# Kernel tuning notes

Measured on AMD Instinct MI355X. Metric: run time of the kernel, lower is better.

## Reference

```python
import jax, jax.numpy as jnp
import numpy as np

SCALE = 1.0 / 16.0      # spatial scale: image coords -> feature-map coords (stride-16 backbone)
OUT = 7                 # roi_pool_outsize
RATIO = 2               # sampling_ratio
NUM_CLASSES = 21
HID = 1024
SCORE_THRESH = 0.05
NMS_THRESH = 0.5
DET = 100               # detections_per_img
MIN_SIZE = 0.01
LOG_MAX = float(np.log(1000.0 / 16.0))  # standard bbox decode dw/dh clamp


def _bilinear(feat, ys, xs):
    # feat [C,H,W]; ys [Py], xs [Px] -> [C,Py,Px] (torchvision roi_align interpolation, aligned=False)
    C, H, W = feat.shape
    vy = (ys > -1.0) & (ys < H)
    vx = (xs > -1.0) & (xs < W)
    y = jnp.clip(ys, 0.0, H - 1.0)
    x = jnp.clip(xs, 0.0, W - 1.0)
    y0 = jnp.floor(y).astype(jnp.int32)
    x0 = jnp.floor(x).astype(jnp.int32)
    y1 = jnp.minimum(y0 + 1, H - 1)
    x1 = jnp.minimum(x0 + 1, W - 1)
    ly = (y - y0)[:, None]
    lx = (x - x0)[None, :]
    f00 = feat[:, y0[:, None], x0[None, :]]
    f01 = feat[:, y0[:, None], x1[None, :]]
    f10 = feat[:, y1[:, None], x0[None, :]]
    f11 = feat[:, y1[:, None], x1[None, :]]
    val = (f00 * (1.0 - ly) * (1.0 - lx) + f01 * (1.0 - ly) * lx
           + f10 * ly * (1.0 - lx) + f11 * ly * lx)
    return val * (vy[:, None] & vx[None, :])


def _roi_align(features, boxes, bidx):
    # features [N,C,H,W], boxes [R,4] (image coords), bidx [R] -> [R,C,OUT,OUT]
    N, C, H, W = features.shape
    b = boxes * SCALE
    rw = jnp.maximum(b[:, 2] - b[:, 0], 1.0)
    rh = jnp.maximum(b[:, 3] - b[:, 1], 1.0)
    bw = rw / OUT
    bh = rh / OUT
    # per-bin sample offsets: (ph + (i+0.5)/ratio) for ph in [0,OUT), i in [0,RATIO)
    g = (jnp.arange(OUT, dtype=jnp.float32)[:, None]
         + (jnp.arange(RATIO, dtype=jnp.float32)[None, :] + 0.5) / RATIO).reshape(-1)  # [OUT*RATIO]
    ys = b[:, 1][:, None] + g[None, :] * bh[:, None]  # [R, OUT*RATIO]
    xs = b[:, 0][:, None] + g[None, :] * bw[:, None]
    vals = jax.vmap(lambda i, yr, xr: _bilinear(features[i], yr, xr))(bidx, ys, xs)  # [R,C,P,P]
    R = boxes.shape[0]
    return vals.reshape(R, C, OUT, RATIO, OUT, RATIO).mean(axis=(3, 5))


def _decode(deltas, props):
    # deltas [R,K,4], props [R,4]; weights (10,10,5,5) as in the module
    pw = props[:, 2] - props[:, 0]
    ph = props[:, 3] - props[:, 1]
    pcx = props[:, 0] + 0.5 * pw
    pcy = props[:, 1] + 0.5 * ph
    dx = deltas[..., 0] / 10.0
    dy = deltas[..., 1] / 10.0
    dw = jnp.minimum(deltas[..., 2] / 5.0, LOG_MAX)
    dh = jnp.minimum(deltas[..., 3] / 5.0, LOG_MAX)
    cx = dx * pw[:, None] + pcx[:, None]
    cy = dy * ph[:, None] + pcy[:, None]
    w = jnp.exp(dw) * pw[:, None]
    h = jnp.exp(dh) * ph[:, None]
    return jnp.stack([cx - 0.5 * w, cy - 0.5 * h, cx + 0.5 * w, cy + 0.5 * h], axis=-1)


def _per_image(scores, boxes, img):
    # scores [S,K], boxes [S,K,4]. Drop background class, flatten, filter, class-aware NMS, top-DET.
    S, K = scores.shape
    sc = scores[:, 1:].reshape(-1)                 # [M]
    bx = boxes[:, 1:, :].reshape(-1, 4)            # [M,4]
    lb = jnp.broadcast_to(jnp.arange(1, K, dtype=jnp.int32)[None, :], (S, K - 1)).reshape(-1)
    wv = bx[:, 2] - bx[:, 0]
    hv = bx[:, 3] - bx[:, 1]
    valid = (sc > SCORE_THRESH) & (wv >= MIN_SIZE) & (hv >= MIN_SIZE)
    live0 = jnp.where(valid, sc, -1.0)
    # batched_nms via per-class coordinate offsets
    nb = bx + (lb.astype(bx.dtype) * (img + 1.0))[:, None]
    areas = (nb[:, 2] - nb[:, 0]) * (nb[:, 3] - nb[:, 1])

    def step(live, _):
        i = jnp.argmax(live)
        s = live[i]
        b = nb[i]
        xx1 = jnp.maximum(b[0], nb[:, 0])
        yy1 = jnp.maximum(b[1], nb[:, 1])
        xx2 = jnp.minimum(b[2], nb[:, 2])
        yy2 = jnp.minimum(b[3], nb[:, 3])
        inter = jnp.maximum(xx2 - xx1, 0.0) * jnp.maximum(yy2 - yy1, 0.0)
        area_i = (b[2] - b[0]) * (b[3] - b[1])
        iou = inter / (area_i + areas - inter + 1e-9)
        live = jnp.where(iou > NMS_THRESH, -1.0, live)  # also suppresses i itself (iou=1)
        return live, (i, s)

    _, (idxs, svals) = jax.lax.scan(step, live0, None, length=DET)
    keep = svals > SCORE_THRESH
    out_boxes = jnp.where(keep[:, None], bx[idxs], 0.0)
    out_scores = jnp.where(keep, svals, 0.0)
    out_labels = jnp.where(keep, lb[idxs], 0)
    return out_boxes, out_scores, out_labels


def _forward(features, proposals, w1, b1, w2, b2, wc, bc, wb, bb, image_size):
    N, C, H, W = features.shape
    S = proposals.shape[1]
    props = proposals.reshape(-1, 4)
    bidx = jnp.repeat(jnp.arange(N), S)
    feats = _roi_align(features, props, bidx)          # [R,C,7,7]
    x = feats.reshape(N * S, -1)                       # [R, C*49]
    h = jax.nn.relu(x @ w1 + b1)
    h = jax.nn.relu(h @ w2 + b2)
    cls = h @ wc + bc                                  # [R,K]
    deltas = (h @ wb + bb).reshape(N * S, NUM_CLASSES, 4)
    scores = jax.nn.softmax(cls, axis=-1)
    boxes = _decode(deltas, props)                     # [R,K,4]
    img = float(image_size)
    boxes = jnp.clip(boxes, 0.0, img)                  # square image -> clip both coords to [0,img]
    scores = scores.reshape(N, S, NUM_CLASSES)
    boxes = boxes.reshape(N, S, NUM_CLASSES, 4)
    return jax.vmap(lambda s, bx: _per_image(s, bx, img))(scores, boxes)


def setup_inputs() -> dict:
    key = jax.random.key(0)
    ks = jax.random.split(key, 12)
    N, S, C, H, W = 2, 512, 512, 50, 50
    IMG = 800
    features = jax.random.normal(ks[0], (N, C, H, W), jnp.float32)
    x1 = jax.random.uniform(ks[1], (N, S)) * (IMG - 80.0)
    y1 = jax.random.uniform(ks[2], (N, S)) * (IMG - 80.0)
    x2 = jnp.minimum(x1 + 16.0 + jax.random.uniform(ks[3], (N, S)) * 180.0, float(IMG))
    y2 = jnp.minimum(y1 + 16.0 + jax.random.uniform(ks[4], (N, S)) * 180.0, float(IMG))
    proposals = jnp.stack([x1, y1, x2, y2], axis=-1)
    D = C * OUT * OUT  # 25088
    w1 = jax.random.normal(ks[5], (D, HID), jnp.float32) * 0.01
    b1 = jnp.zeros((HID,), jnp.float32)
    w2 = jax.random.normal(ks[6], (HID, HID), jnp.float32) * 0.02
    b2 = jnp.zeros((HID,), jnp.float32)
    wc = jax.random.normal(ks[7], (HID, NUM_CLASSES), jnp.float32) * 0.05
    bc = jnp.zeros((NUM_CLASSES,), jnp.float32)
    wb = jax.random.normal(ks[8], (HID, NUM_CLASSES * 4), jnp.float32) * 0.02
    bb = jnp.zeros((NUM_CLASSES * 4,), jnp.float32)
    return {"features": features, "proposals": proposals, "w1": w1, "b1": b1,
            "w2": w2, "b2": b2, "wc": wc, "bc": bc, "wb": wb, "bb": bb,
            "image_size": IMG}


def reference(features, proposals, w1, b1, w2, b2, wc, bc, wb, bb, image_size):
    boxes, scores, labels = _forward(features, proposals, w1, b1, w2, b2, wc, bc, wb, bb, image_size)
    return boxes, scores, labels
```

## Files before the change

kernel.cpp:

```cpp
#include <hip/hip_runtime.h>
#include <cmath>

#define NIMG 2
#define SPROP 512
#define NROI 1024
#define CCH 512
#define FH 50
#define FW 50
#define K1 25088
#define HID 1024
#define NCLS 21
#define NDET 100
#define IMGSZ 800.0f
#define LOGMAX 4.135166556742356f
#define MCAND 10240
#define ZSPLIT 8
#define KCHUNK 3136
#define ZSPLIT2 8
#define KCHUNK2 128

typedef unsigned short u16;
typedef __attribute__((ext_vector_type(8))) short short8;
typedef __attribute__((ext_vector_type(4))) float f32x4;
typedef __attribute__((ext_vector_type(16))) float f32x16;

__device__ __forceinline__ u16 f2bf(float x) {
  unsigned int u = __float_as_uint(x);
  u += 0x7fffu + ((u >> 16) & 1u);
  return (u16)(u >> 16);
}
__device__ __forceinline__ float bf2f(u16 h) {
  return __uint_as_float(((unsigned int)h) << 16);
}

template <bool BF16OUT>
__global__ __launch_bounds__(256) void roi_kernel(
    const float* __restrict__ feat, const float* __restrict__ props,
    float* __restrict__ X, u16* __restrict__ Xhi, u16* __restrict__ Xlo) {
  const int r = blockIdx.x;
  const int n = r >> 9;
  const int tid = threadIdx.x;
  __shared__ float tile[32 * 273 + 16];
  __shared__ float4 ymeta[14];
  __shared__ float4 xmeta[14];
  __shared__ int smin[2];

  const float p0 = props[r * 4 + 0] * 0.0625f;
  const float p1 = props[r * 4 + 1] * 0.0625f;
  const float p2 = props[r * 4 + 2] * 0.0625f;
  const float p3 = props[r * 4 + 3] * 0.0625f;
  const float bw = fmaxf(p2 - p0, 1.0f) / 7.0f;
  const float bh = fmaxf(p3 - p1, 1.0f) / 7.0f;

  if (tid < 14) {
    const int j = tid;
    const float g = (float)(j >> 1) + ((float)(j & 1) + 0.5f) * 0.5f;
    const float y = p1 + g * bh;
    const float vy = (y > -1.0f && y < (float)FH) ? 0.5f : 0.0f;
    const float yc = fminf(fmaxf(y, 0.0f), (float)(FH - 1));
    const int y0 = (int)floorf(yc);
    const int y1 = min(y0 + 1, FH - 1);
    const float ly = yc - (float)y0;
    const float yc0 = fminf(fmaxf(p1 + 0.25f * bh, 0.0f), (float)(FH - 1));
    const int ymin = (int)floorf(yc0);
    float4 m;
    m.x = __int_as_float((y0 - ymin) * 17);
    m.y = __int_as_float((y1 - ymin) * 17);
    m.z = (1.0f - ly) * vy;
    m.w = ly * vy;
    ymeta[j] = m;
    if (j == 0) smin[0] = ymin;
  } else if (tid >= 16 && tid < 30) {
    const int j = tid - 16;
    const float g = (float)(j >> 1) + ((float)(j & 1) + 0.5f) * 0.5f;
    const float x = p0 + g * bw;
    const float vx = (x > -1.0f && x < (float)FW) ? 0.5f : 0.0f;
    const float xc = fminf(fmaxf(x, 0.0f), (float)(FW - 1));
    const int x0 = (int)floorf(xc);
    const int x1 = min(x0 + 1, FW - 1);
    const float lx = xc - (float)x0;
    const float xc0 = fminf(fmaxf(p0 + 0.25f * bw, 0.0f), (float)(FW - 1));
    const int xmin = (int)floorf(xc0);
    const float wx0 = (1.0f - lx) * vx;
    const float wx1 = lx * vx;
    const int d = x1 - x0;
    float4 m;
    m.x = __int_as_float(x0 - xmin);
    m.y = wx0 + (d ? 0.0f : wx1);
    m.z = d ? wx1 : 0.0f;
    m.w = 0.0f;
    xmeta[j] = m;
    if (j == 0) smin[1] = xmin;
  }
  __syncthreads();

  const int ymin = smin[0], xmin = smin[1];
  const float* fb = feat + (size_t)n * CCH * (FH * FW);
  const int gy = min(ymin + (tid >> 4), FH - 1);
  const int gx = min(xmin + (tid & 15), FW - 1);
  const int offp = gy * FW + gx;
  const int wslot = (tid >> 4) * 17 + (tid & 15);
  const int q = tid & 7;
  const int c = tid >> 3;
  const int cb = c * 273;

  float pf[32];
#pragma unroll
  for (int e = 0; e < 32; ++e) pf[e] = fb[(size_t)e * (FH * FW) + offp];

  for (int cc = 0; cc < 16; ++cc) {
#pragma unroll
    for (int e = 0; e < 32; ++e) tile[e * 273 + wslot] = pf[e];
    __syncthreads();
    if (cc < 15) {
      const float* fb2 = fb + (size_t)(cc + 1) * 32 * (FH * FW);
#pragma unroll
      for (int e = 0; e < 32; ++e) pf[e] = fb2[(size_t)e * (FH * FW) + offp];
    }
#pragma unroll
    for (int jj = 0; jj < 7; ++jj) {
      const int s = q + (jj << 3);
      if (s < 49) {
        const int oy = s / 7;
        const int ox = s - oy * 7;
        const float4 ym0 = ymeta[2 * oy];
        const float4 ym1 = ymeta[2 * oy + 1];
        const float4 xm0 = xmeta[2 * ox];
        const float4 xm1 = xmeta[2 * ox + 1];
        float acc = 0.0f;
#pragma unroll
        for (int sy = 0; sy < 2; ++sy) {
          const float4 ym = sy ? ym1 : ym0;
          const int ro0 = cb + __float_as_int(ym.x);
          const int ro1 = cb + __float_as_int(ym.y);
#pragma unroll
          for (int sx = 0; sx < 2; ++sx) {
            const float4 xm = sx ? xm1 : xm0;
            const int px = __float_as_int(xm.x);
            const float a0 = tile[ro0 + px];
            const float a1 = tile[ro0 + px + 1];
            const float b0 = tile[ro1 + px];
            const float b1 = tile[ro1 + px + 1];
            acc += ym.z * (xm.y * a0 + xm.z * a1) +
                   ym.w * (xm.y * b0 + xm.z * b1);
          }
        }
        const size_t k = (size_t)r * K1 + (size_t)(cc * 32 + c) * 49 + s;
        if (BF16OUT) {
          const u16 h = f2bf(acc);
          Xhi[k] = h;
          Xlo[k] = f2bf(acc - bf2f(h));
        } else {
          X[k] = acc;
        }
      }
    }
    __syncthreads();
  }
}

template <int KDIM>
__global__ __launch_bounds__(256) void convw_kernel(
    const float* __restrict__ w, u16* __restrict__ Wh, u16* __restrict__ Wl) {
  __shared__ u16 sh[64][65], sl[64][65];
  const int k0 = blockIdx.x * 64;
  const int n0 = blockIdx.y * 64;
  const int t = threadIdx.x;
#pragma unroll
  for (int e = 0; e < 16; ++e) {
    const int idx = t + e * 256;
    const int kl = idx >> 6, nl = idx & 63;
    const float v = w[(size_t)(k0 + kl) * HID + n0 + nl];
    const u16 h = f2bf(v);
    sh[kl][nl] = h;
    sl[kl][nl] = f2bf(v - bf2f(h));
  }
  __syncthreads();
#pragma unroll
  for (int e = 0; e < 16; ++e) {
    const int idx = t + e * 256;
    const int nl = idx >> 6, kl = idx & 63;
    Wh[(size_t)(n0 + nl) * KDIM + k0 + kl] = sh[kl][nl];
    Wl[(size_t)(n0 + nl) * KDIM + k0 + kl] = sl[kl][nl];
  }
}

template <int KS, int KCH, bool SWZ>
__global__ __launch_bounds__(512, 2) void gemm_mfma_split(
    const u16* __restrict__ Ahg, const u16* __restrict__ Alg,
    const u16* __restrict__ Bhg, const u16* __restrict__ Blg,
    float* __restrict__ CP) {
  __shared__ u16 Ah[128][32], Al[128][32], Bh[256][32], Bl[256][32];
  const int tid = threadIdx.x;
  const int lane = tid & 63;
  const int wv = tid >> 6;
  const int wm = (wv >> 2) << 6;
  const int wn = (wv & 3) << 6;

  int bx = blockIdx.x, by = blockIdx.y, bz = blockIdx.z;
  if (SWZ) {
    const int f = blockIdx.x + ((blockIdx.y + (blockIdx.z << 3)) << 2);
    bz = f & 7;
    const int u = f >> 3;
    bx = u & 3;
    by = u >> 2;
  }
  const int mT = by << 7;
  const int nT = bx << 8;
  const int kz = bz * KCH;
  const int kend = kz + KCH;

  const int sr = tid >> 2;
  const int sq = (tid & 3) << 3;
  const int scw = (((tid & 3) ^ ((sr >> 1) & 3)) << 3);
  const size_t aoff  = (size_t)(mT + sr) * KS + sq;
  const size_t b0off = (size_t)(nT + sr) * KS + sq;
  const size_t b1off = (size_t)(nT + sr + 128) * KS + sq;

  f32x16 acc[2][2];
#pragma unroll
  for (int i = 0; i < 2; ++i)
#pragma unroll
    for (int j = 0; j < 2; ++j)
#pragma unroll
      for (int e = 0; e < 16; ++e) acc[i][j][e] = 0.0f;

  const int fm = lane & 31;
  const int fh = lane >> 5;
  const int vswz = (fm >> 1) & 3;

  uint4 rA  = *(const uint4*)(Ahg + aoff + kz);
  uint4 rL  = *(const uint4*)(Alg + aoff + kz);
  uint4 rB0 = *(const uint4*)(Bhg + b0off + kz);
  uint4 rB1 = *(const uint4*)(Bhg + b1off + kz);
  uint4 rM0 = *(const uint4*)(Blg + b0off + kz);
  uint4 rM1 = *(const uint4*)(Blg + b1off + kz);
  uint4 sA  = *(const uint4*)(Ahg + aoff + kz + 32);
  uint4 sL  = *(const uint4*)(Alg + aoff + kz + 32);
  uint4 sB0 = *(const uint4*)(Bhg + b0off + kz + 32);
  uint4 sB1 = *(const uint4*)(Bhg + b1off + kz + 32);
  uint4 sM0 = *(const uint4*)(Blg + b0off + kz + 32);
  uint4 sM1 = *(const uint4*)(Blg + b1off + kz + 32);

  auto compute = [&]() {
#pragma unroll
    for (int kh = 0; kh < 2; ++kh) {
      const int cA = ((((kh << 1) | fh) ^ vswz) << 3);
      short8 fa_h[2], fa_l[2], fb_h[2], fb_l[2];
#pragma unroll
      for (int t = 0; t < 2; ++t) {
        fa_h[t] = *(const short8*)(&Ah[wm + t * 32 + fm][cA]);
        fa_l[t] = *(const short8*)(&Al[wm + t * 32 + fm][cA]);
        fb_h[t] = *(const short8*)(&Bh[wn + t * 32 + fm][cA]);
        fb_l[t] = *(const short8*)(&Bl[wn + t * 32 + fm][cA]);
      }
#pragma unroll
      for (int ti = 0; ti < 2; ++ti)
#pragma unroll
        for (int tj = 0; tj < 2; ++tj) {
          acc[ti][tj] = __builtin_amdgcn_mfma_f32_32x32x16_bf16(
              fa_h[ti], fb_h[tj], acc[ti][tj], 0, 0, 0);
          acc[ti][tj] = __builtin_amdgcn_mfma_f32_32x32x16_bf16(
              fa_h[ti], fb_l[tj], acc[ti][tj], 0, 0, 0);
          acc[ti][tj] = __builtin_amdgcn_mfma_f32_32x32x16_bf16(
              fa_l[ti], fb_h[tj], acc[ti][tj], 0, 0, 0);
        }
    }
  };

  for (int kb = kz; kb < kend; kb += 64) {
    *(uint4*)(&Ah[sr][scw]) = rA;
    *(uint4*)(&Al[sr][scw]) = rL;
    *(uint4*)(&Bh[sr][scw]) = rB0;
    *(uint4*)(&Bh[sr + 128][scw]) = rB1;
    *(uint4*)(&Bl[sr][scw]) = rM0;
    *(uint4*)(&Bl[sr + 128][scw]) = rM1;
    __syncthreads();
    const int kn1 = (kb + 64 < kend) ? kb + 64 : kz;
    rA  = *(const uint4*)(Ahg + aoff + kn1);
    rL  = *(const uint4*)(Alg + aoff + kn1);
    rB0 = *(const uint4*)(Bhg + b0off + kn1);
    rB1 = *(const uint4*)(Bhg + b1off + kn1);
    rM0 = *(const uint4*)(Blg + b0off + kn1);
    rM1 = *(const uint4*)(Blg + b1off + kn1);
    compute();
    __syncthreads();
    *(uint4*)(&Ah[sr][scw]) = sA;
    *(uint4*)(&Al[sr][scw]) = sL;
    *(uint4*)(&Bh[sr][scw]) = sB0;
    *(uint4*)(&Bh[sr + 128][scw]) = sB1;
    *(uint4*)(&Bl[sr][scw]) = sM0;
    *(uint4*)(&Bl[sr + 128][scw]) = sM1;
    __syncthreads();
    const int kn2 = (kb + 96 < kend) ? kb + 96 : kz;
    sA  = *(const uint4*)(Ahg + aoff + kn2);
    sL  = *(const uint4*)(Alg + aoff + kn2);
    sB0 = *(const uint4*)(Bhg + b0off + kn2);
    sB1 = *(const uint4*)(Bhg + b1off + kn2);
    sM0 = *(const uint4*)(Blg + b0off + kn2);
    sM1 = *(const uint4*)(Blg + b1off + kn2);
    compute();
    __syncthreads();
  }

  float* Cp = CP + (size_t)bz * ((size_t)NROI * HID);
  const int ccol = nT + wn + fm;
  const int rbase = mT + wm + (fh << 2);
#pragma unroll
  for (int ti = 0; ti < 2; ++ti)
#pragma unroll
    for (int tj = 0; tj < 2; ++tj)
#pragma unroll
      for (int rg = 0; rg < 16; ++rg) {
        const int row = rbase + ti * 32 + (rg & 3) + 8 * (rg >> 2);
        Cp[(size_t)row * HID + ccol + tj * 32] = acc[ti][tj][rg];
      }
}

__global__ __launch_bounds__(256) void gemm1_kernel(
    const float* __restrict__ A, const float* __restrict__ B,
    float* __restrict__ CP) {
  __shared__ float As[16][68];
  __shared__ float Bs[16][68];
  const int tid = threadIdx.x;
  const int mTile = blockIdx.y << 6;
  const int nTile = blockIdx.x << 6;
  const int k0 = blockIdx.z * KCHUNK;
  const int ty = tid >> 4, tx = tid & 15;
  const int ar = tid >> 2, ac = (tid & 3) << 2;
  const int br = tid >> 4, bcl = (tid & 15) << 2;
  float acc[4][4] = {};

  for (int kb = k0; kb < k0 + KCHUNK; kb += 16) {
    const float4 av = *(const float4*)(A + (size_t)(mTile + ar) * K1 + kb + ac);
    const float4 bv = *(const float4*)(B + (size_t)(kb + br) * HID + nTile + bcl);
    As[ac + 0][ar] = av.x; As[ac + 1][ar] = av.y;
    As[ac + 2][ar] = av.z; As[ac + 3][ar] = av.w;
    *(float4*)(&Bs[br][bcl]) = bv;
    __syncthreads();
#pragma unroll
    for (int kk = 0; kk < 16; ++kk) {
      const float4 a4 = *(const float4*)(&As[kk][ty << 2]);
      const float4 b4 = *(const float4*)(&Bs[kk][tx << 2]);
      const float aa[4] = {a4.x, a4.y, a4.z, a4.w};
      const float bb4[4] = {b4.x, b4.y, b4.z, b4.w};
#pragma unroll
      for (int i = 0; i < 4; ++i)
#pragma unroll
        for (int j = 0; j < 4; ++j)
          acc[i][j] = fmaf(aa[i], bb4[j], acc[i][j]);
    }
    __syncthreads();
  }
  float* Cp = CP + (size_t)blockIdx.z * (HID * NROI);
#pragma unroll
  for (int i = 0; i < 4; ++i) {
    *(float4*)(Cp + (size_t)(mTile + (ty << 2) + i) * HID + nTile + (tx << 2)) =
        make_float4(acc[i][0], acc[i][1], acc[i][2], acc[i][3]);
  }
}

__global__ __launch_bounds__(256) void bias_relu_bf16_kernel(
    const float* __restrict__ CP, const float* __restrict__ b1,
    u16* __restrict__ H1h, u16* __restrict__ H1l) {
  const int idx = blockIdx.x * 256 + threadIdx.x;
  float v = b1[idx & (HID - 1)];
#pragma unroll
  for (int z = 0; z < ZSPLIT; ++z) v += CP[(size_t)z * (HID * NROI) + idx];
  v = fmaxf(v, 0.0f);
  const u16 h = f2bf(v);
  H1h[idx] = h;
  H1l[idx] = f2bf(v - bf2f(h));
}

__global__ __launch_bounds__(256) void bias_relu_f32_kernel(
    const float* __restrict__ CP, const float* __restrict__ b1,
    float* __restrict__ H1) {
  const int idx = blockIdx.x * 256 + threadIdx.x;
  float v = b1[idx & (HID - 1)];
#pragma unroll
  for (int z = 0; z < ZSPLIT; ++z) v += CP[(size_t)z * (HID * NROI) + idx];
  H1[idx] = fmaxf(v, 0.0f);
}

__global__ __launch_bounds__(256) void bias_relu2_kernel(
    const float* __restrict__ CP2, const float* __restrict__ b2,
    float* __restrict__ H2) {
  const int idx = blockIdx.x * 256 + threadIdx.x;
  float v = b2[idx & (HID - 1)];
#pragma unroll
  for (int z = 0; z < ZSPLIT2; ++z) v += CP2[(size_t)z * (HID * NROI) + idx];
  H2[idx] = fmaxf(v, 0.0f);
}

__global__ __launch_bounds__(256) void gemm2_kernel(
    const float* __restrict__ A, const float* __restrict__ B,
    const float* __restrict__ bias, float* __restrict__ C) {
  __shared__ float As[16][68];
  __shared__ float Bs[16][68];
  const int tid = threadIdx.x;
  const int mTile = blockIdx.y << 6;
  const int nTile = blockIdx.x << 6;
  const int ty = tid >> 4, tx = tid & 15;
  const int ar = tid >> 2, ac = (tid & 3) << 2;
  const int br = tid >> 4, bcl = (tid & 15) << 2;
  float acc[4][4] = {};

  for (int kb = 0; kb < HID; kb += 16) {
    const float4 av = *(const float4*)(A + (size_t)(mTile + ar) * HID + kb + ac);
    const float4 bv = *(const float4*)(B + (size_t)(kb + br) * HID + nTile + bcl);
    As[ac + 0][ar] = av.x; As[ac + 1][ar] = av.y;
    As[ac + 2][ar] = av.z; As[ac + 3][ar] = av.w;
    *(float4*)(&Bs[br][bcl]) = bv;
    __syncthreads();
#pragma unroll
    for (int kk = 0; kk < 16; ++kk) {
      const float4 a4 = *(const float4*)(&As[kk][ty << 2]);
      const float4 b4 = *(const float4*)(&Bs[kk][tx << 2]);
      const float aa[4] = {a4.x, a4.y, a4.z, a4.w};
      const float bb4[4] = {b4.x, b4.y, b4.z, b4.w};
#pragma unroll
      for (int i = 0; i < 4; ++i)
#pragma unroll
        for (int j = 0; j < 4; ++j)
          acc[i][j] = fmaf(aa[i], bb4[j], acc[i][j]);
    }
    __syncthreads();
  }
#pragma unroll
  for (int i = 0; i < 4; ++i) {
#pragma unroll
    for (int j = 0; j < 4; ++j) {
      float v = acc[i][j] + bias[nTile + (tx << 2) + j];
      acc[i][j] = fmaxf(v, 0.0f);
    }
    *(float4*)(C + (size_t)(mTile + (ty << 2) + i) * HID + nTile + (tx << 2)) =
        make_float4(acc[i][0], acc[i][1], acc[i][2], acc[i][3]);
  }
}

__global__ __launch_bounds__(128) void heads_kernel(
    const float* __restrict__ H2m, const float* __restrict__ wc,
    const float* __restrict__ bc, const float* __restrict__ wb,
    const float* __restrict__ bb, const float* __restrict__ props,
    float* __restrict__ BX2, float* __restrict__ NB2,
    float* __restrict__ LV2) {
  const int r = blockIdx.x;
  const int tid = threadIdx.x;
  __shared__ float hrow[HID];
  __shared__ float vals[112];
  __shared__ float red[2];

  for (int i = tid; i < HID; i += 128) hrow[i] = H2m[(size_t)r * HID + i];
  __syncthreads();

  if (tid < 105) {
    float acc;
    if (tid < NCLS) {
      acc = bc[tid];
      for (int kk = 0; kk < HID; ++kk) acc = fmaf(hrow[kk], wc[kk * NCLS + tid], acc);
    } else {
      const int j = tid - NCLS;
      acc = bb[j];
      for (int kk = 0; kk < HID; ++kk) acc = fmaf(hrow[kk], wb[kk * (NCLS * 4) + j], acc);
    }
    vals[tid] = acc;
  }
  __syncthreads();

  if (tid == 0) {
    float m = vals[0];
    for (int k = 1; k < NCLS; ++k) m = fmaxf(m, vals[k]);
    float s = 0.0f;
    for (int k = 0; k < NCLS; ++k) s += expf(vals[k] - m);
    red[0] = m;
    red[1] = 1.0f / s;
  }
  __syncthreads();

  if (tid >= 1 && tid <= 20) {
    const int k = tid;
    const float prob = expf(vals[k] - red[0]) * red[1];

    const float px1 = props[r * 4 + 0], py1 = props[r * 4 + 1];
    const float px2 = props[r * 4 + 2], py2 = props[r * 4 + 3];
    const float pw = px2 - px1, ph = py2 - py1;
    const float pcx = px1 + 0.5f * pw, pcy = py1 + 0.5f * ph;

    const float dx = vals[NCLS + k * 4 + 0] / 10.0f;
    const float dy = vals[NCLS + k * 4 + 1] / 10.0f;
    const float dw = fminf(vals[NCLS + k * 4 + 2] / 5.0f, LOGMAX);
    const float dh = fminf(vals[NCLS + k * 4 + 3] / 5.0f, LOGMAX);

    const float cx = dx * pw + pcx, cy = dy * ph + pcy;
    const float w = expf(dw) * pw, h = expf(dh) * ph;
    float b0 = cx - 0.5f * w, b1c = cy - 0.5f * h;
    float b2 = cx + 0.5f * w, b3 = cy + 0.5f * h;
    b0 = fminf(fmaxf(b0, 0.0f), IMGSZ);
    b1c = fminf(fmaxf(b1c, 0.0f), IMGSZ);
    b2 = fminf(fmaxf(b2, 0.0f), IMGSZ);
    b3 = fminf(fmaxf(b3, 0.0f), IMGSZ);

    const float wv = b2 - b0, hv = b3 - b1c;
    const bool valid = (prob > 0.05f) && (wv >= 0.01f) && (hv >= 0.01f);

    const int n = r >> 9, s = r & 511;
    const int cand = (k - 1) * SPROP + s;
    const size_t bi = (size_t)n * MCAND + cand;
    const float off = (float)k * (IMGSZ + 1.0f);

    BX2[bi * 4 + 0] = b0; BX2[bi * 4 + 1] = b1c;
    BX2[bi * 4 + 2] = b2; BX2[bi * 4 + 3] = b3;
    NB2[bi * 4 + 0] = b0 + off; NB2[bi * 4 + 1] = b1c + off;
    NB2[bi * 4 + 2] = b2 + off; NB2[bi * 4 + 3] = b3 + off;
    LV2[bi] = valid ? prob : -1.0f;
  }
}

template <int CTRL>
__device__ __forceinline__ void red2(float& v, int& ix) {
  const float tv = __int_as_float(__builtin_amdgcn_update_dpp(
      (int)0xC0000000, __float_as_int(v), CTRL, 0xf, 0xf, false));
  const int ti = __builtin_amdgcn_update_dpp(0x7fffffff, ix, CTRL, 0xf, 0xf, false);
  if (tv > v || (tv == v && ti < ix)) { v = tv; ix = ti; }
}
__device__ __forceinline__ void wave_red2(float& v, int& ix) {
  red2<0x111>(v, ix);
  red2<0x112>(v, ix);
  red2<0x114>(v, ix);
  red2<0x118>(v, ix);
  red2<0x142>(v, ix);
  red2<0x143>(v, ix);
}

__global__ __launch_bounds__(64) void nms_class_kernel(
    const float* __restrict__ NB2, const float* __restrict__ LV2,
    float* __restrict__ ksg, int* __restrict__ kig, int* __restrict__ cntg) {
  const int bid = blockIdx.x;
  const int lane = threadIdx.x;
  __shared__ float4 lbox[SPROP];
  const size_t cb = (size_t)bid * SPROP;

  float lv[8], b0[8], b1[8], b2[8], b3[8], ar[8];
#pragma unroll
  for (int j = 0; j < 8; ++j) {
    const int s = lane + j * 64;
    lv[j] = LV2[cb + s];
    const float4 b = *(const float4*)(NB2 + (cb + s) * 4);
    b0[j] = b.x; b1[j] = b.y; b2[j] = b.z; b3[j] = b.w;
    ar[j] = (b.z - b.x) * (b.w - b.y);
    lbox[s] = b;
  }

  int cnt = 0;
  for (int d = 0; d < NDET; ++d) {
    float bv = -2.0f;
    int bix = 0x7fffffff;
#pragma unroll
    for (int j = 0; j < 8; ++j) {
      if (lv[j] > bv) { bv = lv[j]; bix = lane + j * 64; }
    }
    wave_red2(bv, bix);
    const float bv2 = __shfl(bv, 63);
    const int bix2 = __shfl(bix, 63);
    if (bv2 <= 0.05f) break;

    if (lane == 0) {
      ksg[bid * NDET + cnt] = bv2;
      kig[bid * NDET + cnt] = bix2;
    }
    ++cnt;

    const float4 wb = lbox[bix2];
    const float wa = (wb.z - wb.x) * (wb.w - wb.y);
#pragma unroll
    for (int j = 0; j < 8; ++j) {
      const float xx1 = fmaxf(wb.x, b0[j]);
      const float yy1 = fmaxf(wb.y, b1[j]);
      const float xx2 = fminf(wb.z, b2[j]);
      const float yy2 = fminf(wb.w, b3[j]);
      const float inter = fmaxf(xx2 - xx1, 0.0f) * fmaxf(yy2 - yy1, 0.0f);
      const float iou = inter / (wa + ar[j] - inter + 1e-9f);
      if (iou > 0.5f) lv[j] = -1.0f;
    }
  }
  if (lane == 0) cntg[bid] = cnt;
}

__global__ __launch_bounds__(1024) void nms_merge_kernel(
    const float* __restrict__ ksg, const int* __restrict__ kig,
    const int* __restrict__ cntg, const float* __restrict__ BX2,
    float* __restrict__ out) {
  const int n = blockIdx.x;
  const int tid = threadIdx.x;
  __shared__ int cbase[21];
  __shared__ unsigned long long keys[2000];
  __shared__ float ssc[2000];
  __shared__ int sfl[2000];
  __shared__ float svals[NDET];
  __shared__ int sflat[NDET];

  if (tid == 0) {
    int acc = 0;
    for (int c = 0; c < 20; ++c) { cbase[c] = acc; acc += cntg[n * 20 + c]; }
    cbase[20] = acc;
  }
  __syncthreads();
  const int T = cbase[20];

  for (int idx = tid; idx < 20 * NDET; idx += 1024) {
    const int c = idx / NDET, e = idx - (idx / NDET) * NDET;
    if (e < cntg[n * 20 + c]) {
      const int pos = cbase[c] + e;
      const float s = ksg[(n * 20 + c) * NDET + e];
      const int slot = kig[(n * 20 + c) * NDET + e];
      const int flat = slot * 20 + c;
      ssc[pos] = s;
      sfl[pos] = flat;
      keys[pos] = ((unsigned long long)__float_as_uint(s) << 32) |
                  (unsigned long long)(0xFFFFFFFFu - (unsigned)flat);
    }
  }
  __syncthreads();

  float msc[2]; int mfl[2]; unsigned long long mk[2]; int rank[2] = {0, 0};
  bool own[2];
#pragma unroll
  for (int e = 0; e < 2; ++e) {
    const int i = tid + e * 1024;
    own[e] = (i < T);
    if (own[e]) { mk[e] = keys[i]; msc[e] = ssc[i]; mfl[e] = sfl[i]; }
  }
  for (int i = 0; i < T; ++i) {
    const unsigned long long k = keys[i];
    if (own[0] && k > mk[0]) ++rank[0];
    if (own[1] && k > mk[1]) ++rank[1];
  }
#pragma unroll
  for (int e = 0; e < 2; ++e)
    if (own[e] && rank[e] < NDET) { svals[rank[e]] = msc[e]; sflat[rank[e]] = mfl[e]; }
  __syncthreads();

  if (tid < NDET) {
    const int m = (T < NDET) ? T : NDET;
    const bool keep = tid < m;
    float sv = 0.0f;
    float4 bx4 = make_float4(0.0f, 0.0f, 0.0f, 0.0f);
    float label = 0.0f;
    if (keep) {
      sv = svals[tid];
      const int flat = sflat[tid];
      const int c = flat % 20, s = flat / 20;
      bx4 = *(const float4*)(BX2 + ((size_t)(n * 20 + c) * SPROP + s) * 4);
      label = (float)(c + 1);
    }
    out[(n * NDET + tid) * 4 + 0] = bx4.x;
    out[(n * NDET + tid) * 4 + 1] = bx4.y;
    out[(n * NDET + tid) * 4 + 2] = bx4.z;
    out[(n * NDET + tid) * 4 + 3] = bx4.w;
    out[NIMG * NDET * 4 + n * NDET + tid] = sv;
    out[NIMG * NDET * 4 + NIMG * NDET + n * NDET + tid] = label;
  }
}

extern "C" void kernel_launch(void* const* d_in, const int* in_sizes, int n_in,
                              void* d_out, int out_size, void* d_ws, size_t ws_size,
                              hipStream_t stream) {
  const float* features  = (const float*)d_in[0];
  const float* proposals = (const float*)d_in[1];
  const float* w1 = (const float*)d_in[2];
  const float* b1 = (const float*)d_in[3];
  const float* w2 = (const float*)d_in[4];
  const float* b2 = (const float*)d_in[5];
  const float* wc = (const float*)d_in[6];
  const float* bc = (const float*)d_in[7];
  const float* wb = (const float*)d_in[8];
  const float* bb = (const float*)d_in[9];

  const size_t XE = (size_t)NROI * K1;
  const size_t WE = (size_t)K1 * HID;
  const size_t FLOATS_TAIL =
      (size_t)ZSPLIT * NROI * HID + 2 * (size_t)NROI * HID + (size_t)NIMG * MCAND * 10;
  const size_t NEED = (XE * 2 + WE * 2) * sizeof(u16) + FLOATS_TAIL * sizeof(float);

  if (ws_size >= NEED) {
    u16* Xhi = (u16*)d_ws;
    u16* Xlo = Xhi + XE;
    u16* Wh  = Xlo + XE;
    u16* Wl  = Wh + WE;
    float* CP  = (float*)(Wl + WE);
    float* CP2 = CP;
    float* H2  = CP + (size_t)ZSPLIT * NROI * HID;
    float* BX2 = H2 + (size_t)NROI * HID;
    float* NB2 = BX2 + (size_t)NIMG * MCAND * 4;
    float* LV2 = NB2 + (size_t)NIMG * MCAND * 4;
    float* ksg = LV2 + (size_t)NIMG * MCAND;
    int*   kig = (int*)(ksg + (size_t)NIMG * 20 * NDET);
    int*   cntg = kig + (size_t)NIMG * 20 * NDET;
    u16* H1h = Xhi;
    u16* H1l = Xhi + (size_t)NROI * HID;
    u16* W2h = Xlo;
    u16* W2l = Xlo + (size_t)HID * HID;

    convw_kernel<K1><<<dim3(K1 / 64, HID / 64), 256, 0, stream>>>(w1, Wh, Wl);
    roi_kernel<true><<<NROI, 256, 0, stream>>>(features, proposals, nullptr, Xhi, Xlo);
    gemm_mfma_split<K1, KCHUNK, true><<<dim3(4, 8, ZSPLIT), 512, 0, stream>>>(
        Xhi, Xlo, Wh, Wl, CP);
    bias_relu_bf16_kernel<<<(NROI * HID) / 256, 256, 0, stream>>>(CP, b1, H1h, H1l);
    convw_kernel<HID><<<dim3(HID / 64, HID / 64), 256, 0, stream>>>(w2, W2h, W2l);
    gemm_mfma_split<HID, KCHUNK2, true><<<dim3(4, 8, ZSPLIT2), 512, 0, stream>>>(
        H1h, H1l, W2h, W2l, CP2);
    bias_relu2_kernel<<<(NROI * HID) / 256, 256, 0, stream>>>(CP2, b2, H2);
    heads_kernel<<<NROI, 128, 0, stream>>>(H2, wc, bc, wb, bb, proposals,
                                           BX2, NB2, LV2);
    nms_class_kernel<<<NIMG * 20, 64, 0, stream>>>(NB2, LV2, ksg, kig, cntg);
    nms_merge_kernel<<<NIMG, 1024, 0, stream>>>(ksg, kig, cntg, BX2,
                                                (float*)d_out);
  } else {
    float* ws = (float*)d_ws;
    float* X   = ws;
    float* CP  = X + XE;
    float* H1  = CP + (size_t)ZSPLIT * NROI * HID;
    float* H2  = H1 + (size_t)NROI * HID;
    float* BX2 = H2 + (size_t)NROI * HID;
    float* NB2 = BX2 + (size_t)NIMG * MCAND * 4;
    float* LV2 = NB2 + (size_t)NIMG * MCAND * 4;
    float* ksg = LV2 + (size_t)NIMG * MCAND;
    int*   kig = (int*)(ksg + (size_t)NIMG * 20 * NDET);
    int*   cntg = kig + (size_t)NIMG * 20 * NDET;

    roi_kernel<false><<<NROI, 256, 0, stream>>>(features, proposals, X, nullptr, nullptr);
    gemm1_kernel<<<dim3(16, 16, ZSPLIT), 256, 0, stream>>>(X, w1, CP);
    bias_relu_f32_kernel<<<(NROI * HID) / 256, 256, 0, stream>>>(CP, b1, H1);
    gemm2_kernel<<<dim3(16, 16), 256, 0, stream>>>(H1, w2, b2, H2);
    heads_kernel<<<NROI, 128, 0, stream>>>(H2, wc, bc, wb, bb, proposals,
                                           BX2, NB2, LV2);
    nms_class_kernel<<<NIMG * 20, 64, 0, stream>>>(NB2, LV2, ksg, kig, cntg);
    nms_merge_kernel<<<NIMG, 1024, 0, stream>>>(ksg, kig, cntg, BX2,
                                                (float*)d_out);
  }
}
```

Baseline: 792.9 us.

## Stage GEMM tiles with direct global-to-LDS loads into double-buffered shared memory

```diff
diff --git a/kernel.cpp b/kernel.cpp
--- a/kernel.cpp
+++ b/kernel.cpp
@@ -31,6 +31,12 @@
 }
 __device__ __forceinline__ float bf2f(u16 h) {
   return __uint_as_float(((unsigned int)h) << 16);
+}
+
+__device__ __forceinline__ void gld16(const u16* g, u16* l) {
+  __builtin_amdgcn_global_load_lds(
+      (const __attribute__((address_space(1))) void*)g,
+      (__attribute__((address_space(3))) void*)l, 16, 0, 0);
 }
 
 template <bool BF16OUT>
@@ -190,7 +196,8 @@
     const u16* __restrict__ Ahg, const u16* __restrict__ Alg,
     const u16* __restrict__ Bhg, const u16* __restrict__ Blg,
     float* __restrict__ CP) {
-  __shared__ u16 Ah[128][32], Al[128][32], Bh[256][32], Bl[256][32];
+  __shared__ u16 Ah[2][128][32], Al[2][128][32];
+  __shared__ u16 Bh[2][256][32], Bl[2][256][32];
   const int tid = threadIdx.x;
   const int lane = tid & 63;
   const int wv = tid >> 6;
@@ -208,14 +215,14 @@
   const int mT = by << 7;
   const int nT = bx << 8;
   const int kz = bz * KCH;
-  const int kend = kz + KCH;
+  constexpr int NSTEP = KCH / 32;
 
   const int sr = tid >> 2;
-  const int sq = (tid & 3) << 3;
-  const int scw = (((tid & 3) ^ ((sr >> 1) & 3)) << 3);
-  const size_t aoff  = (size_t)(mT + sr) * KS + sq;
-  const size_t b0off = (size_t)(nT + sr) * KS + sq;
-  const size_t b1off = (size_t)(nT + sr + 128) * KS + sq;
+  const int sqw = (((tid & 3) ^ ((tid >> 3) & 3)) << 3);
+  const size_t aoff  = (size_t)(mT + sr) * KS + sqw;
+  const size_t b0off = (size_t)(nT + sr) * KS + sqw;
+  const size_t b1off = (size_t)(nT + sr + 128) * KS + sqw;
+  const int lofs = tid * 8;
 
   f32x16 acc[2][2];
 #pragma unroll
@@ -229,30 +236,26 @@
   const int fh = lane >> 5;
   const int vswz = (fm >> 1) & 3;
 
-  uint4 rA  = *(const uint4*)(Ahg + aoff + kz);
-  uint4 rL  = *(const uint4*)(Alg + aoff + kz);
-  uint4 rB0 = *(const uint4*)(Bhg + b0off + kz);
-  uint4 rB1 = *(const uint4*)(Bhg + b1off + kz);
-  uint4 rM0 = *(const uint4*)(Blg + b0off + kz);
-  uint4 rM1 = *(const uint4*)(Blg + b1off + kz);
-  uint4 sA  = *(const uint4*)(Ahg + aoff + kz + 32);
-  uint4 sL  = *(const uint4*)(Alg + aoff + kz + 32);
-  uint4 sB0 = *(const uint4*)(Bhg + b0off + kz + 32);
-  uint4 sB1 = *(const uint4*)(Bhg + b1off + kz + 32);
-  uint4 sM0 = *(const uint4*)(Blg + b0off + kz + 32);
-  uint4 sM1 = *(const uint4*)(Blg + b1off + kz + 32);
-
-  auto compute = [&]() {
+  auto stage = [&](int buf, int kb) {
+    gld16(Ahg + aoff + kb, &Ah[buf][0][0] + lofs);
+    gld16(Alg + aoff + kb, &Al[buf][0][0] + lofs);
+    gld16(Bhg + b0off + kb, &Bh[buf][0][0] + lofs);
+    gld16(Bhg + b1off + kb, &Bh[buf][128][0] + lofs);
+    gld16(Blg + b0off + kb, &Bl[buf][0][0] + lofs);
+    gld16(Blg + b1off + kb, &Bl[buf][128][0] + lofs);
+  };
+
+  auto compute = [&](int buf) {
 #pragma unroll
     for (int kh = 0; kh < 2; ++kh) {
       const int cA = ((((kh << 1) | fh) ^ vswz) << 3);
       short8 fa_h[2], fa_l[2], fb_h[2], fb_l[2];
 #pragma unroll
       for (int t = 0; t < 2; ++t) {
-        fa_h[t] = *(const short8*)(&Ah[wm + t * 32 + fm][cA]);
-        fa_l[t] = *(const short8*)(&Al[wm + t * 32 + fm][cA]);
-        fb_h[t] = *(const short8*)(&Bh[wn + t * 32 + fm][cA]);
-        fb_l[t] = *(const short8*)(&Bl[wn + t * 32 + fm][cA]);
+        fa_h[t] = *(const short8*)(&Ah[buf][wm + t * 32 + fm][cA]);
+        fa_l[t] = *(const short8*)(&Al[buf][wm + t * 32 + fm][cA]);
+        fb_h[t] = *(const short8*)(&Bh[buf][wn + t * 32 + fm][cA]);
+        fb_l[t] = *(const short8*)(&Bl[buf][wn + t * 32 + fm][cA]);
       }
 #pragma unroll
       for (int ti = 0; ti < 2; ++ti)
@@ -268,39 +271,14 @@
     }
   };
 
-  for (int kb = kz; kb < kend; kb += 64) {
-    *(uint4*)(&Ah[sr][scw]) = rA;
-    *(uint4*)(&Al[sr][scw]) = rL;
-    *(uint4*)(&Bh[sr][scw]) = rB0;
-    *(uint4*)(&Bh[sr + 128][scw]) = rB1;
-    *(uint4*)(&Bl[sr][scw]) = rM0;
-    *(uint4*)(&Bl[sr + 128][scw]) = rM1;
+  stage(0, kz);
+  __syncthreads();
+  int cur = 0;
+  for (int s = 0; s < NSTEP; ++s) {
+    if (s + 1 < NSTEP) stage(cur ^ 1, kz + (s + 1) * 32);
+    compute(cur);
     __syncthreads();
-    const int kn1 = (kb + 64 < kend) ? kb + 64 : kz;
-    rA  = *(const uint4*)(Ahg + aoff + kn1);
-    rL  = *(const uint4*)(Alg + aoff + kn1);
-    rB0 = *(const uint4*)(Bhg + b0off + kn1);
-    rB1 = *(const uint4*)(Bhg + b1off + kn1);
-    rM0 = *(const uint4*)(Blg + b0off + kn1);
-    rM1 = *(const uint4*)(Blg + b1off + kn1);
-    compute();
-    __syncthreads();
-    *(uint4*)(&Ah[sr][scw]) = sA;
-    *(uint4*)(&Al[sr][scw]) = sL;
-    *(uint4*)(&Bh[sr][scw]) = sB0;
-    *(uint4*)(&Bh[sr + 128][scw]) = sB1;
-    *(uint4*)(&Bl[sr][scw]) = sM0;
-    *(uint4*)(&Bl[sr + 128][scw]) = sM1;
-    __syncthreads();
-    const int kn2 = (kb + 96 < kend) ? kb + 96 : kz;
-    sA  = *(const uint4*)(Ahg + aoff + kn2);
-    sL  = *(const uint4*)(Alg + aoff + kn2);
-    sB0 = *(const uint4*)(Bhg + b0off + kn2);
-    sB1 = *(const uint4*)(Bhg + b1off + kn2);
-    sM0 = *(const uint4*)(Blg + b0off + kn2);
-    sM1 = *(const uint4*)(Blg + b1off + kn2);
-    compute();
-    __syncthreads();
+    cur ^= 1;
   }
 
   float* Cp = CP + (size_t)bz * ((size_t)NROI * HID);
```

Result: slower. 823.3 us (+3.8%).
